# Optimization experiments

Hardware: AMD Instinct MI355X
Metric: run time of the kernel (lower is better)

Reference implementation:

```python
import jax, jax.numpy as jnp
import numpy as np

N_NODES = 50000
N_EDGES = 800000
IN_CH = 256
HID = 256
OUT_CH = 128


def setup_inputs() -> dict:
    key = jax.random.key(0)
    ks = jax.random.split(key, 12)
    x = jax.random.normal(ks[0], (N_NODES, IN_CH), dtype=jnp.float32)
    adj_rows = jnp.sort(jax.random.randint(ks[1], (N_EDGES,), 0, N_NODES, dtype=jnp.int32))
    adj_cols = jax.random.randint(ks[2], (N_EDGES,), 0, N_NODES, dtype=jnp.int32)
    # normalized adjacency weights (~1/degree scale)
    adj_vals = jax.random.uniform(ks[3], (N_EDGES,), dtype=jnp.float32) / 16.0
    def xavier(k, fan_in, fan_out):
        lim = float(np.sqrt(6.0 / (fan_in + fan_out)))
        return jax.random.uniform(k, (fan_in, fan_out), dtype=jnp.float32, minval=-lim, maxval=lim)
    Wa0 = xavier(ks[4], IN_CH, HID)
    Wa1 = xavier(ks[5], HID, HID)
    Wl0 = xavier(ks[6], IN_CH + HID, HID)
    Wl1 = xavier(ks[7], 2 * HID, OUT_CH)
    return {
        'x': x, 'adj_rows': adj_rows, 'adj_cols': adj_cols, 'adj_vals': adj_vals,
        'Wa0': Wa0, 'ba0': jnp.zeros((HID,), jnp.float32),
        'Wa1': Wa1, 'ba1': jnp.zeros((HID,), jnp.float32),
        'Wl0': Wl0, 'bl0': jnp.zeros((HID,), jnp.float32),
        'Wl1': Wl1, 'bl1': jnp.zeros((OUT_CH,), jnp.float32),
    }


def reference(x, adj_rows, adj_cols, adj_vals, Wa0, ba0, Wa1, ba1, Wl0, bl0, Wl1, bl1):
    n = x.shape[0]

    def spmm(h):
        # sparse adj @ h : gather neighbor rows, scale by edge weight, segment-sum into dst
        return jax.ops.segment_sum(adj_vals[:, None] * h[adj_cols], adj_rows, num_segments=n)

    # layer 0
    agg = jax.nn.relu(spmm(x) @ Wa0 + ba0)
    h = jax.nn.relu(jnp.concatenate((x, agg), axis=1) @ Wl0 + bl0)
    # layer 1 (last: no activation after linear)
    agg = jax.nn.relu(spmm(h) @ Wa1 + ba1)
    h = jnp.concatenate((h, agg), axis=1) @ Wl1 + bl1
    # F.normalize: row-wise L2 with eps=1e-12
    norm = jnp.maximum(jnp.linalg.norm(h, axis=1, keepdims=True), 1e-12)
    return h / norm
```

## Files before the change

kernel.cpp:

```cpp
#include <hip/hip_runtime.h>

typedef unsigned short u16;
typedef __attribute__((ext_vector_type(8))) __bf16 bf16x8;
typedef __attribute__((ext_vector_type(4))) float f32x4;
typedef __attribute__((ext_vector_type(8))) u16 u16x8;
typedef __attribute__((ext_vector_type(4))) u16 u16x4;

__device__ __forceinline__ float bf2f(u16 u) {
  return __builtin_bit_cast(float, ((unsigned)u) << 16);
}
__device__ __forceinline__ u16 f2bf(float f) {
  unsigned x = __builtin_bit_cast(unsigned, f);
  x += 0x7fffu + ((x >> 16) & 1u);
  return (u16)(x >> 16);
}
__device__ __forceinline__ f32x4 cvt4(u16x4 v) {
  return (f32x4){bf2f(v.x), bf2f(v.y), bf2f(v.z), bf2f(v.w)};
}
__device__ __forceinline__ void gload_lds16(const void* g, void* l) {
  __builtin_amdgcn_global_load_lds(
      (const __attribute__((address_space(1))) void*)g,
      (__attribute__((address_space(3))) void*)l, 16, 0, 0);
}

__global__ void prepw_kernel(const float* __restrict__ W, u16* __restrict__ Wt,
                             int K, int N) {
  int i = blockIdx.x * 256 + threadIdx.x;
  if (i >= K * N) return;
  int k = i / N, n = i - k * N;
  Wt[(size_t)n * K + k] = f2bf(W[i]);
}

__global__ void cvtx_kernel(const float* __restrict__ in, u16* __restrict__ out,
                            int total4) {
  int i = blockIdx.x * 256 + threadIdx.x;
  if (i >= total4) return;
  const float4 v = ((const float4*)in)[i];
  u16x4 o = { f2bf(v.x), f2bf(v.y), f2bf(v.z), f2bf(v.w) };
  ((u16x4*)out)[i] = o;
}

__global__ void rowptr_kernel(const int* __restrict__ rows, int nE,
                              int* __restrict__ rp, int nN) {
  int i = blockIdx.x * 256 + threadIdx.x;
  if (i > nN) return;
  int lo = 0, hi = nE;
  while (lo < hi) { int mid = (lo + hi) >> 1; if (rows[mid] < i) lo = mid + 1; else hi = mid; }
  rp[i] = lo;
}

__global__ __launch_bounds__(256) void spmm_kernel(
    const u16* __restrict__ X, const int* __restrict__ rp,
    const int* __restrict__ cols, const float* __restrict__ vals,
    u16* __restrict__ out, int nN) {
  int lane = threadIdx.x & 63;
  int node = blockIdx.x * 4 + (threadIdx.x >> 6);
  if (node >= nN) return;
  int e0 = rp[node], e1 = rp[node + 1];
  f32x4 s0 = {0.f, 0.f, 0.f, 0.f}, s1 = s0, s2 = s0, s3 = s0;
  const u16* xp = X + (size_t)lane * 4;
  int e = e0;
  for (; e + 4 <= e1; e += 4) {
    int c0 = cols[e], c1 = cols[e + 1], c2 = cols[e + 2], c3 = cols[e + 3];
    float v0 = vals[e], v1 = vals[e + 1], v2 = vals[e + 2], v3 = vals[e + 3];
    u16x4 x0 = *(const u16x4*)(xp + (size_t)c0 * 256);
    u16x4 x1 = *(const u16x4*)(xp + (size_t)c1 * 256);
    u16x4 x2 = *(const u16x4*)(xp + (size_t)c2 * 256);
    u16x4 x3 = *(const u16x4*)(xp + (size_t)c3 * 256);
    s0 += v0 * cvt4(x0);
    s1 += v1 * cvt4(x1);
    s2 += v2 * cvt4(x2);
    s3 += v3 * cvt4(x3);
  }
  for (; e < e1; ++e) {
    int c = cols[e];
    float v = vals[e];
    u16x4 xv = *(const u16x4*)(xp + (size_t)c * 256);
    s0 += v * cvt4(xv);
  }
  f32x4 s = (s0 + s1) + (s2 + s3);
  u16x4 o = { f2bf(s.x), f2bf(s.y), f2bf(s.z), f2bf(s.w) };
  *(u16x4*)(out + (size_t)node * 256 + lane * 4) = o;
}

template<int KTOT, bool SPLIT, bool RELU, bool OUTF32>
__global__ __launch_bounds__(256) void gemm_kernel(
    const u16* __restrict__ A0, const u16* __restrict__ A1,
    const u16* __restrict__ Wt, const float* __restrict__ bias,
    void* __restrict__ outp, int M, int N) {
  __shared__ u16 As[128 * 64];
  __shared__ u16 Bs[128 * 64];

  const int lane = threadIdx.x & 63;
  const int wid = threadIdx.x >> 6;
  const int wr = wid >> 1, wc = wid & 1;
  const int row0b = blockIdx.y * 128;
  const int col0b = blockIdx.x * 128;
  const int lr = lane & 15;
  const int kg = lane >> 4;

  const int u = (wid * 4) * 64 + lane;
  f32x4 acc[4][4];
  #pragma unroll
  for (int ni = 0; ni < 4; ++ni) {
    float bv = bias[col0b + wc * 64 + ni * 16 + lr];
    #pragma unroll
    for (int mi = 0; mi < 4; ++mi) acc[mi][ni] = (f32x4){bv, bv, bv, bv};
  }

  constexpr int KSTEPS = KTOT / 64;
  for (int kt = 0; kt < KSTEPS; ++kt) {
    const u16* Asrc = (!SPLIT || kt < 4) ? A0 : A1;
    const int kkl = (!SPLIT || kt < 4) ? kt * 64 : (kt - 4) * 64;

    if (kt) __syncthreads();
    #pragma unroll
    for (int i = 0; i < 4; ++i) {
      const int c = wid * 4 + i;
      const int uu = u + i * 64;
      const int row = uu >> 3;
      const int ksd = uu & 7;
      const int kss = ksd ^ (row & 7);
      int grow = row0b + row;
      if (grow >= M) grow = M - 1;
      gload_lds16(Asrc + (size_t)grow * 256 + kkl + kss * 8, &As[c * 512]);
      gload_lds16(Wt + (size_t)(col0b + row) * KTOT + kt * 64 + kss * 8, &Bs[c * 512]);
    }
    __syncthreads();

    #pragma unroll
    for (int ks = 0; ks < 2; ++ks) {
      const int q = ks * 4 + kg;
      bf16x8 a[4], b[4];
      #pragma unroll
      for (int mi = 0; mi < 4; ++mi) {
        const int r = wr * 64 + mi * 16 + lr;
        a[mi] = __builtin_bit_cast(bf16x8,
            *(const u16x8*)&As[r * 64 + (q ^ (r & 7)) * 8]);
      }
      #pragma unroll
      for (int ni = 0; ni < 4; ++ni) {
        const int cb = wc * 64 + ni * 16 + lr;
        b[ni] = __builtin_bit_cast(bf16x8,
            *(const u16x8*)&Bs[cb * 64 + (q ^ (cb & 7)) * 8]);
      }
      #pragma unroll
      for (int mi = 0; mi < 4; ++mi)
        #pragma unroll
        for (int ni = 0; ni < 4; ++ni)
          acc[mi][ni] = __builtin_amdgcn_mfma_f32_16x16x32_bf16(a[mi], b[ni], acc[mi][ni], 0, 0, 0);
    }
  }

  #pragma unroll
  for (int mi = 0; mi < 4; ++mi) {
    #pragma unroll
    for (int j = 0; j < 4; ++j) {
      int r = row0b + wr * 64 + mi * 16 + kg * 4 + j;
      if (r >= M) continue;
      #pragma unroll
      for (int ni = 0; ni < 4; ++ni) {
        float v = acc[mi][ni][j];
        if (RELU) v = v > 0.f ? v : 0.f;
        int c = col0b + wc * 64 + ni * 16 + lr;
        if (OUTF32) ((float*)outp)[(size_t)r * N + c] = v;
        else        ((u16*)outp)[(size_t)r * N + c] = f2bf(v);
      }
    }
  }
}

__global__ __launch_bounds__(256) void norm_kernel(const float* __restrict__ h2,
                                                   float* __restrict__ out, int nN) {
  int lane = threadIdx.x & 63;
  int node = blockIdx.x * 4 + (threadIdx.x >> 6);
  if (node >= nN) return;
  const float2 v = *(const float2*)(h2 + (size_t)node * 128 + lane * 2);
  float ss = v.x * v.x + v.y * v.y;
  #pragma unroll
  for (int m = 1; m < 64; m <<= 1) ss += __shfl_xor(ss, m, 64);
  float nrm = sqrtf(ss);
  nrm = nrm > 1e-12f ? nrm : 1e-12f;
  float inv = 1.f / nrm;
  float2 o = { v.x * inv, v.y * inv };
  *(float2*)(out + (size_t)node * 128 + lane * 2) = o;
}

extern "C" void kernel_launch(void* const* d_in, const int* in_sizes, int n_in,
                              void* d_out, int out_size, void* d_ws, size_t ws_size,
                              hipStream_t stream) {
  const float* x        = (const float*)d_in[0];
  const int*   adj_rows = (const int*)d_in[1];
  const int*   adj_cols = (const int*)d_in[2];
  const float* adj_vals = (const float*)d_in[3];
  const float* Wa0 = (const float*)d_in[4];
  const float* ba0 = (const float*)d_in[5];
  const float* Wa1 = (const float*)d_in[6];
  const float* ba1 = (const float*)d_in[7];
  const float* Wl0 = (const float*)d_in[8];
  const float* bl0 = (const float*)d_in[9];
  const float* Wl1 = (const float*)d_in[10];
  const float* bl1 = (const float*)d_in[11];

  const int nN = in_sizes[0] / 256;
  const int nE = in_sizes[1];

  char* ws = (char*)d_ws;
  size_t off = 0;
  auto alloc = [&](size_t bytes) -> void* {
    void* p = ws + off;
    off += (bytes + 255) & ~(size_t)255;
    return p;
  };
  u16* x_bf  = (u16*)alloc((size_t)nN * 256 * 2);
  u16* aggA  = (u16*)alloc((size_t)nN * 256 * 2);
  u16* aggB  = (u16*)alloc((size_t)nN * 256 * 2);
  u16* h_bf  = (u16*)alloc((size_t)nN * 256 * 2);
  int* rp    = (int*)alloc((size_t)(nN + 1) * 4);
  u16* wt_a0 = (u16*)alloc(256 * 256 * 2);
  u16* wt_a1 = (u16*)alloc(256 * 256 * 2);
  u16* wt_l0 = (u16*)alloc(512 * 256 * 2);
  u16* wt_l1 = (u16*)alloc(512 * 128 * 2);
  float* h2  = (float*)aggA;
  if (off > ws_size) return;

  dim3 blk(256);
  prepw_kernel<<<dim3((256 * 256 + 255) / 256), blk, 0, stream>>>(Wa0, wt_a0, 256, 256);
  prepw_kernel<<<dim3((256 * 256 + 255) / 256), blk, 0, stream>>>(Wa1, wt_a1, 256, 256);
  prepw_kernel<<<dim3((512 * 256 + 255) / 256), blk, 0, stream>>>(Wl0, wt_l0, 512, 256);
  prepw_kernel<<<dim3((512 * 128 + 255) / 256), blk, 0, stream>>>(Wl1, wt_l1, 512, 128);
  cvtx_kernel<<<dim3((nN * 64 + 255) / 256), blk, 0, stream>>>(x, x_bf, nN * 64);
  rowptr_kernel<<<dim3((nN + 1 + 255) / 256), blk, 0, stream>>>(adj_rows, nE, rp, nN);

  const int MB = (nN + 127) / 128;
  dim3 gN256(2, MB);
  dim3 gN128(1, MB);
  dim3 gNode((nN + 3) / 4);

  spmm_kernel<<<gNode, blk, 0, stream>>>(x_bf, rp, adj_cols, adj_vals, aggA, nN);
  gemm_kernel<256, false, true, false><<<gN256, blk, 0, stream>>>(aggA, nullptr, wt_a0, ba0, aggB, nN, 256);
  gemm_kernel<512, true, true, false><<<gN256, blk, 0, stream>>>(x_bf, aggB, wt_l0, bl0, h_bf, nN, 256);
  spmm_kernel<<<gNode, blk, 0, stream>>>(h_bf, rp, adj_cols, adj_vals, aggA, nN);
  gemm_kernel<256, false, true, false><<<gN256, blk, 0, stream>>>(aggA, nullptr, wt_a1, ba1, aggB, nN, 256);
  gemm_kernel<512, true, false, true><<<gN128, blk, 0, stream>>>(h_bf, aggB, wt_l1, bl1, h2, nN, 128);
  norm_kernel<<<gNode, blk, 0, stream>>>(h2, (float*)d_out, nN);
}
```

Before: 234.9 us.

## Fuse L2 normalize into final GEMM, batch weight prep, widen spmm gather

```diff
diff --git a/kernel.cpp b/kernel.cpp
--- a/kernel.cpp
+++ b/kernel.cpp
@@ -23,12 +23,19 @@
       (__attribute__((address_space(3))) void*)l, 16, 0, 0);
 }
 
-__global__ void prepw_kernel(const float* __restrict__ W, u16* __restrict__ Wt,
-                             int K, int N) {
+__global__ void prepw4_kernel(const float* __restrict__ W0, u16* __restrict__ T0,
+                              const float* __restrict__ W1, u16* __restrict__ T1,
+                              const float* __restrict__ W2, u16* __restrict__ T2,
+                              const float* __restrict__ W3, u16* __restrict__ T3) {
   int i = blockIdx.x * 256 + threadIdx.x;
-  if (i >= K * N) return;
+  const float* W; u16* T; int K, N;
+  if (i < 65536)        { W = W0; T = T0; K = 256; N = 256; }
+  else if (i < 131072)  { W = W1; T = T1; K = 256; N = 256; i -= 65536; }
+  else if (i < 262144)  { W = W2; T = T2; K = 512; N = 256; i -= 131072; }
+  else if (i < 327680)  { W = W3; T = T3; K = 512; N = 128; i -= 262144; }
+  else return;
   int k = i / N, n = i - k * N;
-  Wt[(size_t)n * K + k] = f2bf(W[i]);
+  T[(size_t)n * K + k] = f2bf(W[i]);
 }
 
 __global__ void cvtx_kernel(const float* __restrict__ in, u16* __restrict__ out,
@@ -57,39 +64,40 @@
   int node = blockIdx.x * 4 + (threadIdx.x >> 6);
   if (node >= nN) return;
   int e0 = rp[node], e1 = rp[node + 1];
-  f32x4 s0 = {0.f, 0.f, 0.f, 0.f}, s1 = s0, s2 = s0, s3 = s0;
+  f32x4 s[8];
+  #pragma unroll
+  for (int i = 0; i < 8; ++i) s[i] = (f32x4){0.f, 0.f, 0.f, 0.f};
   const u16* xp = X + (size_t)lane * 4;
-  int e = e0;
-  for (; e + 4 <= e1; e += 4) {
-    int c0 = cols[e], c1 = cols[e + 1], c2 = cols[e + 2], c3 = cols[e + 3];
-    float v0 = vals[e], v1 = vals[e + 1], v2 = vals[e + 2], v3 = vals[e + 3];
-    u16x4 x0 = *(const u16x4*)(xp + (size_t)c0 * 256);
-    u16x4 x1 = *(const u16x4*)(xp + (size_t)c1 * 256);
-    u16x4 x2 = *(const u16x4*)(xp + (size_t)c2 * 256);
-    u16x4 x3 = *(const u16x4*)(xp + (size_t)c3 * 256);
-    s0 += v0 * cvt4(x0);
-    s1 += v1 * cvt4(x1);
-    s2 += v2 * cvt4(x2);
-    s3 += v3 * cvt4(x3);
-  }
-  for (; e < e1; ++e) {
-    int c = cols[e];
-    float v = vals[e];
-    u16x4 xv = *(const u16x4*)(xp + (size_t)c * 256);
-    s0 += v * cvt4(xv);
-  }
-  f32x4 s = (s0 + s1) + (s2 + s3);
-  u16x4 o = { f2bf(s.x), f2bf(s.y), f2bf(s.z), f2bf(s.w) };
+  const int elast = e1 - 1;
+  for (int base = e0; base < e1; base += 16) {
+    int c[16]; float v[16];
+    #pragma unroll
+    for (int i = 0; i < 16; ++i) {
+      int idx = base + i;
+      bool ok = idx < e1;
+      int j = ok ? idx : elast;
+      c[i] = cols[j];
+      v[i] = ok ? vals[j] : 0.f;
+    }
+    u16x4 xv[16];
+    #pragma unroll
+    for (int i = 0; i < 16; ++i) xv[i] = *(const u16x4*)(xp + (size_t)c[i] * 256);
+    #pragma unroll
+    for (int i = 0; i < 16; ++i) s[i & 7] += v[i] * cvt4(xv[i]);
+  }
+  f32x4 t = ((s[0] + s[1]) + (s[2] + s[3])) + ((s[4] + s[5]) + (s[6] + s[7]));
+  u16x4 o = { f2bf(t.x), f2bf(t.y), f2bf(t.z), f2bf(t.w) };
   *(u16x4*)(out + (size_t)node * 256 + lane * 4) = o;
 }
 
-template<int KTOT, bool SPLIT, bool RELU, bool OUTF32>
+template<int KTOT, bool SPLIT, bool RELU, bool OUTF32, bool NORM>
 __global__ __launch_bounds__(256) void gemm_kernel(
     const u16* __restrict__ A0, const u16* __restrict__ A1,
     const u16* __restrict__ Wt, const float* __restrict__ bias,
     void* __restrict__ outp, int M, int N) {
   __shared__ u16 As[128 * 64];
   __shared__ u16 Bs[128 * 64];
+  __shared__ float red[128][2];
 
   const int lane = threadIdx.x & 63;
   const int wid = threadIdx.x >> 6;
@@ -152,6 +160,36 @@
     }
   }
 
+  float invn[4][4];
+  if (NORM) {
+    #pragma unroll
+    for (int mi = 0; mi < 4; ++mi) {
+      #pragma unroll
+      for (int j = 0; j < 4; ++j) {
+        float p = 0.f;
+        #pragma unroll
+        for (int ni = 0; ni < 4; ++ni) { float v = acc[mi][ni][j]; p += v * v; }
+        #pragma unroll
+        for (int m = 1; m < 16; m <<= 1) p += __shfl_xor(p, m, 64);
+        int rl = wr * 64 + mi * 16 + kg * 4 + j;
+        if (lr == 0) red[rl][wc] = p;
+        invn[mi][j] = 0.f;
+      }
+    }
+    __syncthreads();
+    #pragma unroll
+    for (int mi = 0; mi < 4; ++mi) {
+      #pragma unroll
+      for (int j = 0; j < 4; ++j) {
+        int rl = wr * 64 + mi * 16 + kg * 4 + j;
+        float ss = red[rl][0] + red[rl][1];
+        float nrm = sqrtf(ss);
+        nrm = nrm > 1e-12f ? nrm : 1e-12f;
+        invn[mi][j] = 1.f / nrm;
+      }
+    }
+  }
+
   #pragma unroll
   for (int mi = 0; mi < 4; ++mi) {
     #pragma unroll
@@ -162,28 +200,13 @@
       for (int ni = 0; ni < 4; ++ni) {
         float v = acc[mi][ni][j];
         if (RELU) v = v > 0.f ? v : 0.f;
+        if (NORM) v *= invn[mi][j];
         int c = col0b + wc * 64 + ni * 16 + lr;
         if (OUTF32) ((float*)outp)[(size_t)r * N + c] = v;
         else        ((u16*)outp)[(size_t)r * N + c] = f2bf(v);
       }
     }
   }
-}
-
-__global__ __launch_bounds__(256) void norm_kernel(const float* __restrict__ h2,
-                                                   float* __restrict__ out, int nN) {
-  int lane = threadIdx.x & 63;
-  int node = blockIdx.x * 4 + (threadIdx.x >> 6);
-  if (node >= nN) return;
-  const float2 v = *(const float2*)(h2 + (size_t)node * 128 + lane * 2);
-  float ss = v.x * v.x + v.y * v.y;
-  #pragma unroll
-  for (int m = 1; m < 64; m <<= 1) ss += __shfl_xor(ss, m, 64);
-  float nrm = sqrtf(ss);
-  nrm = nrm > 1e-12f ? nrm : 1e-12f;
-  float inv = 1.f / nrm;
-  float2 o = { v.x * inv, v.y * inv };
-  *(float2*)(out + (size_t)node * 128 + lane * 2) = o;
 }
 
 extern "C" void kernel_launch(void* const* d_in, const int* in_sizes, int n_in,
@@ -221,14 +244,10 @@
   u16* wt_a1 = (u16*)alloc(256 * 256 * 2);
   u16* wt_l0 = (u16*)alloc(512 * 256 * 2);
   u16* wt_l1 = (u16*)alloc(512 * 128 * 2);
-  float* h2  = (float*)aggA;
   if (off > ws_size) return;
 
   dim3 blk(256);
-  prepw_kernel<<<dim3((256 * 256 + 255) / 256), blk, 0, stream>>>(Wa0, wt_a0, 256, 256);
-  prepw_kernel<<<dim3((256 * 256 + 255) / 256), blk, 0, stream>>>(Wa1, wt_a1, 256, 256);
-  prepw_kernel<<<dim3((512 * 256 + 255) / 256), blk, 0, stream>>>(Wl0, wt_l0, 512, 256);
-  prepw_kernel<<<dim3((512 * 128 + 255) / 256), blk, 0, stream>>>(Wl1, wt_l1, 512, 128);
+  prepw4_kernel<<<dim3(1280), blk, 0, stream>>>(Wa0, wt_a0, Wa1, wt_a1, Wl0, wt_l0, Wl1, wt_l1);
   cvtx_kernel<<<dim3((nN * 64 + 255) / 256), blk, 0, stream>>>(x, x_bf, nN * 64);
   rowptr_kernel<<<dim3((nN + 1 + 255) / 256), blk, 0, stream>>>(adj_rows, nE, rp, nN);
 
@@ -238,10 +257,9 @@
   dim3 gNode((nN + 3) / 4);
 
   spmm_kernel<<<gNode, blk, 0, stream>>>(x_bf, rp, adj_cols, adj_vals, aggA, nN);
-  gemm_kernel<256, false, true, false><<<gN256, blk, 0, stream>>>(aggA, nullptr, wt_a0, ba0, aggB, nN, 256);
-  gemm_kernel<512, true, true, false><<<gN256, blk, 0, stream>>>(x_bf, aggB, wt_l0, bl0, h_bf, nN, 256);
+  gemm_kernel<256, false, true, false, false><<<gN256, blk, 0, stream>>>(aggA, nullptr, wt_a0, ba0, aggB, nN, 256);
+  gemm_kernel<512, true, true, false, false><<<gN256, blk, 0, stream>>>(x_bf, aggB, wt_l0, bl0, h_bf, nN, 256);
   spmm_kernel<<<gNode, blk, 0, stream>>>(h_bf, rp, adj_cols, adj_vals, aggA, nN);
-  gemm_kernel<256, false, true, false><<<gN256, blk, 0, stream>>>(aggA, nullptr, wt_a1, ba1, aggB, nN, 256);
-  gemm_kernel<512, true, false, true><<<gN128, blk, 0, stream>>>(h_bf, aggB, wt_l1, bl1, h2, nN, 128);
-  norm_kernel<<<gNode, blk, 0, stream>>>(h2, (float*)d_out, nN);
-}
+  gemm_kernel<256, false, true, false, false><<<gN256, blk, 0, stream>>>(aggA, nullptr, wt_a1, ba1, aggB, nN, 256);
+  gemm_kernel<512, true, false, true, true><<<gN128, blk, 0, stream>>>(h_bf, aggB, wt_l1, bl1, (float*)d_out, nN, 128);
+}
```

Measured after the change: 242.6 us. 3.3% more time.
